# Optimization experiments

Measured on AMD Instinct MI355X. Metric: run time of the kernel, lower is better.

Reference implementation:

```python
import jax, jax.numpy as jnp
import numpy as np

N, T, D = 2, 4096, 1024
H, E, L = 8, 4, 32
DK, DV = 64, 64

def setup_inputs():
    key = jax.random.key(0)
    ks = jax.random.split(key, 8)
    def randw(k, *d):
        return jax.random.normal(k, d, dtype=jnp.float32) / np.float32(np.sqrt(d[-1]))
    return {
        "X": jax.random.normal(ks[0], (N, T, D), dtype=jnp.float32),
        "w_G": randw(ks[1], H, E, D),
        "b_G": jnp.full((H, E), -float(H) ** 0.5, dtype=jnp.float32),
        "w_K": randw(ks[2], H, DK, D),
        "w_V": randw(ks[3], H, DV, D),
        "w_Q": randw(ks[4], H, DK, D),
        "w_O": randw(ks[5], DV * H, D),
        "init_K_rec": randw(ks[6], E, L, DK),
        "init_V_rec": randw(ks[7], E, L, DV),
    }

def _pscan(A, Xv, Y0):
    # Y_t = A_t * Y_{t-1} + X_t along axis 3 (chunk index), Y_{-1} = Y0
    Ae = jnp.broadcast_to(A[..., None], Xv.shape)
    Xv = Xv.at[..., 0, :].add(A[..., 0, None] * Y0)
    def op(c1, c2):
        a1, x1 = c1
        a2, x2 = c2
        return a1 * a2, a2 * x1 + x2
    _, Y = jax.lax.associative_scan(op, (Ae, Xv), axis=3)
    return Y

def reference(X, w_G, b_G, w_K, w_V, w_Q, w_O, init_K_rec, init_V_rec):
    n, t, _ = X.shape
    t_pad = ((t - 1) // L + 1) * L
    Xp = jnp.pad(X, ((0, 0), (0, t_pad - t), (0, 0)))
    # gates and projections
    G = jax.nn.sigmoid(jnp.einsum('ntd,hed->nhet', Xp, w_G) + b_G[None, :, :, None])
    K = jnp.einsum('ntc,hdc->nhtd', Xp, w_K)
    V = jnp.einsum('ntc,hdc->nhtd', Xp, w_V)
    A = 1.0 - jnp.minimum(G.sum(axis=1), 1.0)               # [n, E, t_pad]
    gK = jnp.einsum('nhet,nhtd->netd', G, K)
    gV = jnp.einsum('nhet,nhtd->netd', G, V)
    # split time as (L, t_pad//L): outer dim L, scan over chunk index (matches torch unflatten(2,(L,-1)))
    tc = t_pad // L
    A = A.reshape(n, E, L, tc)
    gK = gK.reshape(n, E, L, tc, DK)
    gV = gV.reshape(n, E, L, tc, DV)
    iK = jnp.broadcast_to(init_K_rec[None], (n, E, L, DK))
    iV = jnp.broadcast_to(init_V_rec[None], (n, E, L, DV))
    nK = _pscan(A, gK, iK).reshape(n, E, t_pad, DK)
    nV = _pscan(A, gV, iV).reshape(n, E, t_pad, DV)
    recK = jnp.concatenate([iK, nK], axis=2)                 # [n, E, L+t_pad, DK]
    recV = jnp.concatenate([iV, nV], axis=2)
    # moving window of size L ending at current position (slice starts at index 1 of rec buffer)
    idx = 1 + jnp.arange(t_pad)[:, None] + jnp.arange(L)[None, :]
    uk = recK[:, :, idx]                                     # [n, E, t_pad, L, DK]
    uv = recV[:, :, idx]                                     # [n, E, t_pad, L, DV]
    Q = jnp.einsum('ntc,hdc->nhtd', Xp, w_Q)
    scores = jnp.einsum('nhtd,netld->nhtel', Q, uk) / jnp.float32(np.sqrt(DK))
    probs = jax.nn.softmax(scores.reshape(n, H, t_pad, E * L), axis=-1).reshape(scores.shape)
    Y = jnp.einsum('nhtel,netld->nthd', probs, uv).reshape(n, t_pad, H * DV)
    return (Y @ w_O)[:, :t]
```

## Files before the change

kernel.cpp:

```cpp
#include <hip/hip_runtime.h>
#include <hip/hip_bf16.h>


using f4 = float4;
typedef __attribute__((ext_vector_type(8))) short short8;
typedef __attribute__((ext_vector_type(4))) float floatx4;

__device__ __forceinline__ ushort f2bf(float x) {
  unsigned u = __float_as_uint(x);
  u += 0x7fffu + ((u >> 16) & 1u);
  return (ushort)(u >> 16);
}
__device__ __forceinline__ unsigned pk2(float lo, float hi) {
  return (unsigned)f2bf(lo) | ((unsigned)f2bf(hi) << 16);
}

__device__ __forceinline__ void gll16(const void* g, void* l) {
  __builtin_amdgcn_global_load_lds((const __attribute__((address_space(1))) void*)g,
                                   (__attribute__((address_space(3))) void*)l, 16, 0, 0);
}

__global__ __launch_bounds__(256)
void conv_f32_bf16(const float* __restrict__ src, ushort* __restrict__ dst, int n4) {
  for (int i = blockIdx.x * blockDim.x + threadIdx.x; i < n4; i += gridDim.x * blockDim.x) {
    f4 v = ((const f4*)src)[i];
    ushort4 o; o.x = f2bf(v.x); o.y = f2bf(v.y); o.z = f2bf(v.z); o.w = f2bf(v.w);
    ((ushort4*)dst)[i] = o;
  }
}

__global__ __launch_bounds__(256)
void conv_weights(const float* __restrict__ wK, const float* __restrict__ wV,
                  const float* __restrict__ wQ, const float* __restrict__ wG,
                  ushort* __restrict__ wAll) {
  int i4 = blockIdx.x * 256 + threadIdx.x;
  int idx = i4 * 4;
  int row = idx >> 10;
  f4 v = make_float4(0.f, 0.f, 0.f, 0.f);
  if (row < 512)       v = *(const f4*)&wK[idx];
  else if (row < 1024) v = *(const f4*)&wV[idx - 524288];
  else if (row < 1536) v = *(const f4*)&wQ[idx - 1048576];
  else if (row < 1568) v = *(const f4*)&wG[idx - 1572864];
  ushort4 o; o.x = f2bf(v.x); o.y = f2bf(v.y); o.z = f2bf(v.z); o.w = f2bf(v.w);
  *(ushort4*)&wAll[idx] = o;
}

__global__ __launch_bounds__(256)
void transpose_wO(const float* __restrict__ wO, ushort* __restrict__ wObf) {
  int i = blockIdx.x * 256 + threadIdx.x;
  int n = i >> 9, k = i & 511;
  wObf[i] = f2bf(wO[(size_t)k * 1024 + n]);
}

#define PROJ_STEP(KT, WAITS, STAGE_) do {                                        \
  asm volatile("s_waitcnt vmcnt(" WAITS ")" ::: "memory");                       \
  __builtin_amdgcn_s_barrier();                                                  \
  asm volatile("" ::: "memory");                                                 \
  if (STAGE_) {                                                                  \
    const int k2 = ((KT) + 2) * 32;                                              \
    ushort* la = &As[(((KT) + 2) & 3) * 8192 + tid * 8];                         \
    ushort* lb = &Bs[(((KT) + 2) & 3) * 8192 + tid * 8];                         \
    gll16(gA + k2, la); gll16(gA + 131072 + k2, la + 4096);                      \
    gll16(gB + k2, lb); gll16(gB + 131072 + k2, lb + 4096);                      \
  }                                                                              \
  {                                                                              \
    const int ko = ((KT) & 3) * 8192;                                            \
    short8 bfrag[4];                                                             \
    _Pragma("unroll")                                                            \
    for (int ni = 0; ni < 4; ni++)                                               \
      bfrag[ni] = *(const short8*)(Bf + ko + ni * 512);                          \
    __builtin_amdgcn_s_setprio(1);                                               \
    _Pragma("unroll")                                                            \
    for (int mi = 0; mi < 8; mi++) {                                             \
      short8 afrag = *(const short8*)(Af + ko + mi * 512);                       \
      _Pragma("unroll")                                                          \
      for (int ni = 0; ni < 4; ni++)                                             \
        acc[mi][ni] = __builtin_amdgcn_mfma_f32_16x16x32_bf16(                   \
            afrag, bfrag[ni], acc[mi][ni], 0, 0, 0);                             \
    }                                                                            \
    __builtin_amdgcn_s_setprio(0);                                               \
  }                                                                              \
} while (0)

__global__ __launch_bounds__(512, 2)
void proj_gemm_256(const ushort* __restrict__ Xbf, const ushort* __restrict__ wAll,
                   float* __restrict__ Kp, float* __restrict__ Vp,
                   ushort* __restrict__ Qbf, float* __restrict__ Glin)
{
  __shared__ ushort As[4 * 8192];
  __shared__ ushort Bs[4 * 8192];

  const int tid = threadIdx.x;
  const int bid = blockIdx.x;
  const int xcd = bid & 7, slot = bid >> 3;
  const int ct = slot % 7;
  const int my = xcd * 4 + slot / 7;
  const int m0 = my * 256;
  const int n0 = ct * 256;

  const int lane = tid & 63;
  const int w = tid >> 6;
  const int wm = (w >> 2) * 128;
  const int wn = (w & 3) * 64;
  const int l15 = lane & 15, lg = lane >> 4;

  const int srow = tid >> 2, sc8 = (tid & 3) * 8;
  const ushort* gA = Xbf  + (size_t)(m0 + srow) * 1024 + sc8;
  const ushort* gB = wAll + (size_t)(n0 + srow) * 1024 + sc8;

  const ushort* Af = As + (wm + l15) * 32 + lg * 8;
  const ushort* Bf = Bs + (wn + l15) * 32 + lg * 8;

  floatx4 acc[8][4];
#pragma unroll
  for (int mi = 0; mi < 8; mi++)
#pragma unroll
    for (int ni = 0; ni < 4; ni++) acc[mi][ni] = (floatx4){0.f, 0.f, 0.f, 0.f};

#pragma unroll
  for (int t_ = 0; t_ < 2; t_++) {
    const int k0 = t_ * 32;
    ushort* la = &As[t_ * 8192 + tid * 8];
    ushort* lb = &Bs[t_ * 8192 + tid * 8];
    gll16(gA + k0, la); gll16(gA + 131072 + k0, la + 4096);
    gll16(gB + k0, lb); gll16(gB + 131072 + k0, lb + 4096);
  }

#pragma unroll 1
  for (int kt = 0; kt < 30; ++kt) PROJ_STEP(kt, "4", true);
  PROJ_STEP(30, "4", false);
  PROJ_STEP(31, "0", false);

#pragma unroll
  for (int mi = 0; mi < 8; mi++) {
    const int rm = m0 + wm + mi * 16 + lg * 4;
#pragma unroll
    for (int ni = 0; ni < 4; ni++) {
      const int cn = wn + ni * 16 + l15;
#pragma unroll
      for (int j = 0; j < 4; j++) {
        const float v = acc[mi][ni][j];
        if (ct < 2)      Kp [(size_t)(rm + j) * 512 + ct * 256 + cn] = v;
        else if (ct < 4) Vp [(size_t)(rm + j) * 512 + (ct - 2) * 256 + cn] = v;
        else if (ct < 6) Qbf[(size_t)(rm + j) * 512 + (ct - 4) * 256 + cn] = f2bf(v * 0.125f);
        else if (cn < 32) Glin[(size_t)(rm + j) * 32 + cn] = v;
      }
    }
  }
}

__global__ __launch_bounds__(256)
void out_gemm_mfma(const ushort* __restrict__ Ybf, const ushort* __restrict__ wObf,
                   float* __restrict__ out)
{
  __shared__ ushort As[4096];
  __shared__ ushort Bs[4096];
  const int tid = threadIdx.x;
  const int m0 = blockIdx.y * 128;
  const int n0 = blockIdx.x * 128;
  const int lane = tid & 63;
  const int wv = tid >> 6;
  const int wm = (wv >> 1) * 64, wn = (wv & 1) * 64;

  const int srow = tid >> 2, scol = (tid & 3) * 8;
  const ushort* gA = Ybf  + (size_t)(m0 + srow) * 512 + scol;
  const ushort* gB = wObf + (size_t)(n0 + srow) * 512 + scol;
  ushort* lA0 = &As[tid * 8]; ushort* lA1 = &As[2048 + tid * 8];
  ushort* lB0 = &Bs[tid * 8]; ushort* lB1 = &Bs[2048 + tid * 8];

  floatx4 acc[4][4];
#pragma unroll
  for (int i = 0; i < 4; i++)
#pragma unroll
    for (int j = 0; j < 4; j++) acc[i][j] = (floatx4){0.f, 0.f, 0.f, 0.f};

  const int fr = lane & 15;
  const int fk = (lane >> 4) * 8;
  const short8* pA[4]; const short8* pB[4];
#pragma unroll
  for (int i = 0; i < 4; i++) {
    pA[i] = (const short8*)&As[(wm + i * 16 + fr) * 32 + fk];
    pB[i] = (const short8*)&Bs[(wn + i * 16 + fr) * 32 + fk];
  }

  for (int k0 = 0; k0 < 512; k0 += 32) {
    gll16(gA + k0, lA0);
    gll16(gA + 32768 + k0, lA1);
    gll16(gB + k0, lB0);
    gll16(gB + 32768 + k0, lB1);
    __syncthreads();
    short8 a[4], b[4];
#pragma unroll
    for (int i = 0; i < 4; i++) { a[i] = *pA[i]; b[i] = *pB[i]; }
#pragma unroll
    for (int mi = 0; mi < 4; mi++)
#pragma unroll
      for (int ni = 0; ni < 4; ni++)
        acc[mi][ni] = __builtin_amdgcn_mfma_f32_16x16x32_bf16(a[mi], b[ni], acc[mi][ni], 0, 0, 0);
    __syncthreads();
  }

  const int fq = lane >> 4;
#pragma unroll
  for (int mi = 0; mi < 4; mi++) {
    int rm = m0 + wm + mi * 16 + fq * 4;
#pragma unroll
    for (int ni = 0; ni < 4; ni++) {
      int cn = n0 + wn + ni * 16 + fr;
#pragma unroll
      for (int j = 0; j < 4; j++)
        out[(size_t)(rm + j) * 1024 + cn] = acc[mi][ni][j];
    }
  }
}

__global__ __launch_bounds__(256)
void gate_kernel(const float* __restrict__ Glin, const float* __restrict__ bG,
                 const float* __restrict__ Kp, const float* __restrict__ Vp,
                 float* __restrict__ gK, float* __restrict__ gV, float* __restrict__ Aout)
{
  const int nt = blockIdx.x * 4 + (threadIdx.x >> 6);
  const int lane = threadIdx.x & 63;
  const int n = nt >> 12;
  const int t = nt & 4095;

  float g[32];
  float gsum[4] = {0.f, 0.f, 0.f, 0.f};
#pragma unroll
  for (int f = 0; f < 32; f++) {
    float z = Glin[(size_t)nt * 32 + f] + bG[f];
    float s = 1.f / (1.f + __expf(-z));
    g[f] = s;
    gsum[f & 3] += s;
  }
  if (lane < 4) {
    float a = 1.f - fminf(gsum[lane], 1.f);
    Aout[(size_t)(n * 4 + lane) * 4096 + t] = a;
  }
  float gk[4] = {0.f, 0.f, 0.f, 0.f}, gv[4] = {0.f, 0.f, 0.f, 0.f};
#pragma unroll
  for (int h = 0; h < 8; h++) {
    float kv = Kp[(size_t)nt * 512 + h * 64 + lane];
    float vv = Vp[(size_t)nt * 512 + h * 64 + lane];
#pragma unroll
    for (int e = 0; e < 4; e++) {
      gk[e] = fmaf(g[h * 4 + e], kv, gk[e]);
      gv[e] = fmaf(g[h * 4 + e], vv, gv[e]);
    }
  }
#pragma unroll
  for (int e = 0; e < 4; e++) {
    size_t base = ((size_t)(n * 4 + e) * 4096 + t) * 64 + lane;
    gK[base] = gk[e];
    gV[base] = gv[e];
  }
}

__global__ __launch_bounds__(64)
void scan_kernel(float* __restrict__ gK, float* __restrict__ gV,
                 const float* __restrict__ Aarr,
                 const float* __restrict__ initK, const float* __restrict__ initV)
{
  __shared__ float sB[128 * 64];
  __shared__ float sA[128];
  const int b = blockIdx.x;
  const int half = b >> 8, sub = b & 255;
  float* gX = half ? gV : gK;
  const float* initX = half ? initV : initK;
  const int n = sub >> 7, r = sub & 127, e = r >> 5, l = r & 31;
  const int tbase = l * 128;
  const size_t base = ((size_t)(n * 4 + e) * 4096 + tbase) * 64;
  const int tid = threadIdx.x;

  const f4* src = (const f4*)&gX[base];
#pragma unroll
  for (int q = 0; q < 32; q++)
    *(f4*)&sB[(tid + q * 64) * 4] = src[tid + q * 64];
  sA[tid]      = Aarr[(size_t)(n * 4 + e) * 4096 + tbase + tid];
  sA[64 + tid] = Aarr[(size_t)(n * 4 + e) * 4096 + tbase + 64 + tid];
  __syncthreads();

  float state = initX[((size_t)e * 32 + l) * 64 + tid];
  float* dst = &gX[base];
  for (int c = 0; c < 128; c++) {
    state = fmaf(sA[c], state, sB[c * 64 + tid]);
    dst[c * 64 + tid] = state;
  }
}

__global__ __launch_bounds__(256, 1)
void attn_mfma(const ushort* __restrict__ Qbf, const float* __restrict__ nK,
               const float* __restrict__ nV, const float* __restrict__ initK,
               const float* __restrict__ initV, ushort* __restrict__ Yout)
{
  __shared__ ushort Kw[4][4096];
  __shared__ ushort Vt[4][4096];
  __shared__ ushort Pl[4][4096];

  const int blk = blockIdx.x;
  const int n = blk >> 7, c = blk & 127;
  const int t0 = c * 32;
  const int tid = threadIdx.x;
  const int lane = tid & 63;
  const int w = tid >> 6;
  const int l15 = lane & 15, lg = lane >> 4;

  short8 qf[4][2];
#pragma unroll
  for (int mi = 0; mi < 4; mi++) {
    int m = w * 64 + mi * 16 + l15;
    int t = t0 + (m & 31), h = m >> 5;
    const ushort* src = &Qbf[((size_t)(n * 4096 + t)) * 512 + h * 64];
#pragma unroll
    for (int kk = 0; kk < 2; kk++)
      qf[mi][kk] = *(const short8*)&src[kk * 32 + lg * 8];
  }

#pragma unroll 4
  for (int it = 0; it < 16; it++) {
    int idx = it * 256 + tid;
    int e = idx >> 10, u = (idx >> 4) & 63, d = (idx & 15) * 4;
    int s = t0 - 31 + u;
    int scl = s < 4095 ? s : 4095;
    const float* pK = (s >= 0) ? &nK[(((size_t)(n * 4 + e)) * 4096 + scl) * 64 + d]
                               : &initK[((size_t)e * 32 + (s + 32)) * 64 + d];
    const float* pV = (s >= 0) ? &nV[(((size_t)(n * 4 + e)) * 4096 + scl) * 64 + d]
                               : &initV[((size_t)e * 32 + (s + 32)) * 64 + d];
    f4 kv = *(const f4*)pK;
    f4 vv = *(const f4*)pV;
    if (u == 63) { kv = make_float4(0.f,0.f,0.f,0.f); vv = make_float4(0.f,0.f,0.f,0.f); }
    uint2 kp; kp.x = pk2(kv.x, kv.y); kp.y = pk2(kv.z, kv.w);
    int ka = (u * 128 + d * 2) ^ ((u & 7) << 4);
    *(uint2*)((char*)&Kw[e][0] + ka) = kp;
    ushort vb[4] = { f2bf(vv.x), f2bf(vv.y), f2bf(vv.z), f2bf(vv.w) };
#pragma unroll
    for (int q = 0; q < 4; q++) {
      int dq = d + q;
      int va = (dq * 128 + u * 2) ^ ((dq & 7) << 4);
      *(ushort*)((char*)&Vt[e][0] + va) = vb[q];
    }
  }
  __syncthreads();

  floatx4 Yacc[4][4];
#pragma unroll
  for (int mi = 0; mi < 4; mi++)
#pragma unroll
    for (int nd = 0; nd < 4; nd++) Yacc[mi][nd] = (floatx4){0.f,0.f,0.f,0.f};
  float mrun[4][4], lrun[4][4];
#pragma unroll
  for (int mi = 0; mi < 4; mi++)
#pragma unroll
    for (int r = 0; r < 4; r++) { mrun[mi][r] = -1e30f; lrun[mi][r] = 0.f; }

  const floatx4 zf = (floatx4){0.f,0.f,0.f,0.f};
  char* pb = (char*)&Pl[w][0];

#pragma unroll
  for (int half = 0; half < 2; half++) {
    floatx4 S[2][4][4];
#pragma unroll
    for (int ep = 0; ep < 2; ep++) {
      const int e = half * 2 + ep;
#pragma unroll
      for (int ni = 0; ni < 4; ni++) {
        const int urow = ni * 16 + l15;
        const int sw = (urow & 7) << 4;
        short8 kf0 = *(const short8*)((const char*)&Kw[e][0] + ((urow * 128 + lg * 16) ^ sw));
        short8 kf1 = *(const short8*)((const char*)&Kw[e][0] + ((urow * 128 + 64 + lg * 16) ^ sw));
#pragma unroll
        for (int mi = 0; mi < 4; mi++) {
          floatx4 t_ = __builtin_amdgcn_mfma_f32_16x16x32_bf16(qf[mi][0], kf0, zf, 0, 0, 0);
          S[ep][mi][ni] = __builtin_amdgcn_mfma_f32_16x16x32_bf16(qf[mi][1], kf1, t_, 0, 0, 0);
        }
      }
    }
#pragma unroll
    for (int mi = 0; mi < 4; mi++)
#pragma unroll
      for (int r = 0; r < 4; r++) {
        const int iq = (mi & 1) * 16 + lg * 4 + r;
        float mx = mrun[mi][r];
#pragma unroll
        for (int ep = 0; ep < 2; ep++)
#pragma unroll
          for (int ni = 0; ni < 4; ni++) {
            const int u = ni * 16 + l15;
            float v = ((unsigned)(u - iq) < 32u) ? S[ep][mi][ni][r] : -1e30f;
            S[ep][mi][ni][r] = v;
            mx = fmaxf(mx, v);
          }
        mx = fmaxf(mx, __shfl_xor(mx, 1));
        mx = fmaxf(mx, __shfl_xor(mx, 2));
        mx = fmaxf(mx, __shfl_xor(mx, 4));
        mx = fmaxf(mx, __shfl_xor(mx, 8));
        float sc = __expf(mrun[mi][r] - mx);
        mrun[mi][r] = mx;
        float sum = 0.f;
#pragma unroll
        for (int ep = 0; ep < 2; ep++)
#pragma unroll
          for (int ni = 0; ni < 4; ni++) {
            float p = __expf(S[ep][mi][ni][r] - mx);
            S[ep][mi][ni][r] = p;
            sum += p;
          }
        sum += __shfl_xor(sum, 1);
        sum += __shfl_xor(sum, 2);
        sum += __shfl_xor(sum, 4);
        sum += __shfl_xor(sum, 8);
        lrun[mi][r] = lrun[mi][r] * sc + sum;
#pragma unroll
        for (int nd = 0; nd < 4; nd++) Yacc[mi][nd][r] *= sc;
      }
#pragma unroll
    for (int ep = 0; ep < 2; ep++) {
      const int e = half * 2 + ep;
#pragma unroll
      for (int mi = 0; mi < 4; mi++)
#pragma unroll
        for (int r = 0; r < 4; r++) {
          const int m = mi * 16 + lg * 4 + r;
          const int base = m * 128, sw = (m & 7) << 4;
#pragma unroll
          for (int ni = 0; ni < 4; ni++) {
            const int u = ni * 16 + l15;
            *(ushort*)(pb + ((base + u * 2) ^ sw)) = f2bf(S[ep][mi][ni][r]);
          }
        }
      asm volatile("s_waitcnt lgkmcnt(0)" ::: "memory");
      __builtin_amdgcn_sched_barrier(0);
#pragma unroll
      for (int kk = 0; kk < 2; kk++) {
        short8 pa[4];
#pragma unroll
        for (int mi = 0; mi < 4; mi++) {
          const int m = mi * 16 + l15;
          pa[mi] = *(const short8*)(pb + ((m * 128 + kk * 64 + lg * 16) ^ ((m & 7) << 4)));
        }
#pragma unroll
        for (int nd = 0; nd < 4; nd++) {
          const int dr = nd * 16 + l15;
          short8 vf = *(const short8*)((const char*)&Vt[e][0] +
                        ((dr * 128 + kk * 64 + lg * 16) ^ ((dr & 7) << 4)));
#pragma unroll
          for (int mi = 0; mi < 4; mi++)
            Yacc[mi][nd] = __builtin_amdgcn_mfma_f32_16x16x32_bf16(pa[mi], vf, Yacc[mi][nd], 0, 0, 0);
        }
      }
    }
  }

#pragma unroll
  for (int mi = 0; mi < 4; mi++)
#pragma unroll
    for (int r = 0; r < 4; r++) {
      const float inv = 1.f / lrun[mi][r];
      const int m = w * 64 + mi * 16 + lg * 4 + r;
      const int t = t0 + (m & 31), h = m >> 5;
      ushort* dst = &Yout[((size_t)(n * 4096 + t)) * 512 + h * 64];
#pragma unroll
      for (int nd = 0; nd < 4; nd++)
        dst[nd * 16 + l15] = f2bf(Yacc[mi][nd][r] * inv);
    }
}

extern "C" void kernel_launch(void* const* d_in, const int* in_sizes, int n_in,
                              void* d_out, int out_size, void* d_ws, size_t ws_size,
                              hipStream_t stream) {
  const float* X     = (const float*)d_in[0];
  const float* wG    = (const float*)d_in[1];
  const float* bG    = (const float*)d_in[2];
  const float* wK    = (const float*)d_in[3];
  const float* wV    = (const float*)d_in[4];
  const float* wQ    = (const float*)d_in[5];
  const float* wO    = (const float*)d_in[6];
  const float* initK = (const float*)d_in[7];
  const float* initV = (const float*)d_in[8];
  float* out = (float*)d_out;

  float* ws = (float*)d_ws;
  ushort* Xbf  = (ushort*)(ws + 0);
  float*  gK   = ws + 0;
  float*  gV   = ws + 2097152;
  ushort* wAll = (ushort*)(ws + 4194304);
  ushort* wObf = (ushort*)(ws + 5111808);
  float*  Glin = ws + 5373952;
  float*  Kp   = ws + 5636096;
  ushort* Ybf  = (ushort*)Kp;
  float*  Vp   = ws + 9830400;
  ushort* Qbf  = (ushort*)(ws + 14024704);
  float*  Aarr = ws + 16121856;

  conv_f32_bf16<<<2048, 256, 0, stream>>>(X, Xbf, 2097152);
  conv_weights<<<1792, 256, 0, stream>>>(wK, wV, wQ, wG, wAll);
  transpose_wO<<<2048, 256, 0, stream>>>(wO, wObf);
  proj_gemm_256<<<224, 512, 0, stream>>>(Xbf, wAll, Kp, Vp, Qbf, Glin);
  gate_kernel<<<2048, 256, 0, stream>>>(Glin, bG, Kp, Vp, gK, gV, Aarr);
  scan_kernel<<<512, 64, 0, stream>>>(gK, gV, Aarr, initK, initV);
  attn_mfma<<<256, 256, 0, stream>>>(Qbf, gK, gV, initK, initV, Ybf);
  out_gemm_mfma<<<dim3(8, 64), 256, 0, stream>>>(Ybf, wObf, out);
}
```

Baseline: 222.9 us.

## Deepen projection prefetch to three stages and rewrite output GEMM pipelined

The projection GEMM now prefetches three k-tiles ahead instead of two, using the fourth LDS buffer, with adjusted vmcnt waits. The output GEMM is replaced by a 256x128-tile, 512-thread kernel with a four-buffer global_load_lds pipeline, an XCD-aware block-to-tile mapping and a single barrier per step. Both changes aim to hide global-memory latency behind MFMA work. The cost is more LDS per block and more in-flight loads, which may reduce occupancy.

```diff
diff --git a/kernel.cpp b/kernel.cpp
--- a/kernel.cpp
+++ b/kernel.cpp
@@ -55,13 +55,12 @@
 #define PROJ_STEP(KT, WAITS, STAGE_) do {                                        \
   asm volatile("s_waitcnt vmcnt(" WAITS ")" ::: "memory");                       \
   __builtin_amdgcn_s_barrier();                                                  \
-  asm volatile("" ::: "memory");                                                 \
   if (STAGE_) {                                                                  \
-    const int k2 = ((KT) + 2) * 32;                                              \
-    ushort* la = &As[(((KT) + 2) & 3) * 8192 + tid * 8];                         \
-    ushort* lb = &Bs[(((KT) + 2) & 3) * 8192 + tid * 8];                         \
-    gll16(gA + k2, la); gll16(gA + 131072 + k2, la + 4096);                      \
-    gll16(gB + k2, lb); gll16(gB + 131072 + k2, lb + 4096);                      \
+    const int k3 = ((KT) + 3) * 32;                                              \
+    ushort* la = &As[(((KT) + 3) & 3) * 8192 + tid * 8];                         \
+    ushort* lb = &Bs[(((KT) + 3) & 3) * 8192 + tid * 8];                         \
+    gll16(gA + k3, la); gll16(gA + 131072 + k3, la + 4096);                      \
+    gll16(gB + k3, lb); gll16(gB + 131072 + k3, lb + 4096);                      \
   }                                                                              \
   {                                                                              \
     const int ko = ((KT) & 3) * 8192;                                            \
@@ -118,7 +117,7 @@
     for (int ni = 0; ni < 4; ni++) acc[mi][ni] = (floatx4){0.f, 0.f, 0.f, 0.f};
 
 #pragma unroll
-  for (int t_ = 0; t_ < 2; t_++) {
+  for (int t_ = 0; t_ < 3; t_++) {
     const int k0 = t_ * 32;
     ushort* la = &As[t_ * 8192 + tid * 8];
     ushort* lb = &Bs[t_ * 8192 + tid * 8];
@@ -127,7 +126,8 @@
   }
 
 #pragma unroll 1
-  for (int kt = 0; kt < 30; ++kt) PROJ_STEP(kt, "4", true);
+  for (int kt = 0; kt < 29; ++kt) PROJ_STEP(kt, "8", true);
+  PROJ_STEP(29, "8", false);
   PROJ_STEP(30, "4", false);
   PROJ_STEP(31, "0", false);
 
@@ -149,64 +149,91 @@
   }
 }
 
-__global__ __launch_bounds__(256)
-void out_gemm_mfma(const ushort* __restrict__ Ybf, const ushort* __restrict__ wObf,
-                   float* __restrict__ out)
+#define OUT_STEP(KT, WAITS, STAGE_) do {                                         \
+  asm volatile("s_waitcnt vmcnt(" WAITS ")" ::: "memory");                       \
+  __builtin_amdgcn_s_barrier();                                                  \
+  if (STAGE_) {                                                                  \
+    const int k3 = ((KT) + 3) * 32;                                              \
+    ushort* la = &As[(((KT) + 3) & 3) * 8192 + tid * 8];                         \
+    ushort* lb = &Bs[(((KT) + 3) & 3) * 4096 + tid * 8];                         \
+    gll16(gA + k3, la); gll16(gA + 65536 + k3, la + 4096);                       \
+    gll16(gB + k3, lb);                                                          \
+  }                                                                              \
+  {                                                                              \
+    const int koA = ((KT) & 3) * 8192;                                           \
+    const int koB = ((KT) & 3) * 4096;                                           \
+    short8 bfrag[4];                                                             \
+    _Pragma("unroll")                                                            \
+    for (int ni = 0; ni < 4; ni++)                                               \
+      bfrag[ni] = *(const short8*)(Bf + koB + ni * 512);                         \
+    __builtin_amdgcn_s_setprio(1);                                               \
+    _Pragma("unroll")                                                            \
+    for (int mi = 0; mi < 4; mi++) {                                             \
+      short8 afrag = *(const short8*)(Af + koA + mi * 512);                      \
+      _Pragma("unroll")                                                          \
+      for (int ni = 0; ni < 4; ni++)                                             \
+        acc[mi][ni] = __builtin_amdgcn_mfma_f32_16x16x32_bf16(                   \
+            afrag, bfrag[ni], acc[mi][ni], 0, 0, 0);                             \
+    }                                                                            \
+    __builtin_amdgcn_s_setprio(0);                                               \
+  }                                                                              \
+} while (0)
+
+__global__ __launch_bounds__(512, 2)
+void out_gemm_256(const ushort* __restrict__ Ybf, const ushort* __restrict__ wObf,
+                  float* __restrict__ out)
 {
-  __shared__ ushort As[4096];
-  __shared__ ushort Bs[4096];
+  __shared__ ushort As[4 * 8192];
+  __shared__ ushort Bs[4 * 4096];
+
   const int tid = threadIdx.x;
-  const int m0 = blockIdx.y * 128;
-  const int n0 = blockIdx.x * 128;
+  const int bid = blockIdx.x;
+  const int xcd = bid & 7, slot = bid >> 3;
+  const int ct = slot & 7;
+  const int my = xcd * 4 + (slot >> 3);
+  const int m0 = my * 256;
+  const int n0 = ct * 128;
+
   const int lane = tid & 63;
-  const int wv = tid >> 6;
-  const int wm = (wv >> 1) * 64, wn = (wv & 1) * 64;
-
-  const int srow = tid >> 2, scol = (tid & 3) * 8;
-  const ushort* gA = Ybf  + (size_t)(m0 + srow) * 512 + scol;
-  const ushort* gB = wObf + (size_t)(n0 + srow) * 512 + scol;
-  ushort* lA0 = &As[tid * 8]; ushort* lA1 = &As[2048 + tid * 8];
-  ushort* lB0 = &Bs[tid * 8]; ushort* lB1 = &Bs[2048 + tid * 8];
+  const int w = tid >> 6;
+  const int wm = (w >> 1) * 64;
+  const int wn = (w & 1) * 64;
+  const int l15 = lane & 15, lg = lane >> 4;
+
+  const int srow = tid >> 2, sc8 = (tid & 3) * 8;
+  const ushort* gA = Ybf  + (size_t)(m0 + srow) * 512 + sc8;
+  const ushort* gB = wObf + (size_t)(n0 + srow) * 512 + sc8;
+
+  const ushort* Af = As + (wm + l15) * 32 + lg * 8;
+  const ushort* Bf = Bs + (wn + l15) * 32 + lg * 8;
 
   floatx4 acc[4][4];
 #pragma unroll
-  for (int i = 0; i < 4; i++)
-#pragma unroll
-    for (int j = 0; j < 4; j++) acc[i][j] = (floatx4){0.f, 0.f, 0.f, 0.f};
-
-  const int fr = lane & 15;
-  const int fk = (lane >> 4) * 8;
-  const short8* pA[4]; const short8* pB[4];
-#pragma unroll
-  for (int i = 0; i < 4; i++) {
-    pA[i] = (const short8*)&As[(wm + i * 16 + fr) * 32 + fk];
-    pB[i] = (const short8*)&Bs[(wn + i * 16 + fr) * 32 + fk];
-  }
-
-  for (int k0 = 0; k0 < 512; k0 += 32) {
-    gll16(gA + k0, lA0);
-    gll16(gA + 32768 + k0, lA1);
-    gll16(gB + k0, lB0);
-    gll16(gB + 32768 + k0, lB1);
-    __syncthreads();
-    short8 a[4], b[4];
-#pragma unroll
-    for (int i = 0; i < 4; i++) { a[i] = *pA[i]; b[i] = *pB[i]; }
-#pragma unroll
-    for (int mi = 0; mi < 4; mi++)
-#pragma unroll
-      for (int ni = 0; ni < 4; ni++)
-        acc[mi][ni] = __builtin_amdgcn_mfma_f32_16x16x32_bf16(a[mi], b[ni], acc[mi][ni], 0, 0, 0);
-    __syncthreads();
-  }
-
-  const int fq = lane >> 4;
+  for (int mi = 0; mi < 4; mi++)
+#pragma unroll
+    for (int ni = 0; ni < 4; ni++) acc[mi][ni] = (floatx4){0.f, 0.f, 0.f, 0.f};
+
+#pragma unroll
+  for (int t_ = 0; t_ < 3; t_++) {
+    const int k0 = t_ * 32;
+    ushort* la = &As[t_ * 8192 + tid * 8];
+    ushort* lb = &Bs[t_ * 4096 + tid * 8];
+    gll16(gA + k0, la); gll16(gA + 65536 + k0, la + 4096);
+    gll16(gB + k0, lb);
+  }
+
+#pragma unroll 1
+  for (int kt = 0; kt < 13; ++kt) OUT_STEP(kt, "6", true);
+  OUT_STEP(13, "6", false);
+  OUT_STEP(14, "3", false);
+  OUT_STEP(15, "0", false);
+
 #pragma unroll
   for (int mi = 0; mi < 4; mi++) {
-    int rm = m0 + wm + mi * 16 + fq * 4;
+    const int rm = m0 + wm + mi * 16 + lg * 4;
 #pragma unroll
     for (int ni = 0; ni < 4; ni++) {
-      int cn = n0 + wn + ni * 16 + fr;
+      const int cn = n0 + wn + ni * 16 + l15;
 #pragma unroll
       for (int j = 0; j < 4; j++)
         out[(size_t)(rm + j) * 1024 + cn] = acc[mi][ni][j];
@@ -499,5 +526,5 @@
   gate_kernel<<<2048, 256, 0, stream>>>(Glin, bG, Kp, Vp, gK, gV, Aarr);
   scan_kernel<<<512, 64, 0, stream>>>(gK, gV, Aarr, initK, initV);
   attn_mfma<<<256, 256, 0, stream>>>(Qbf, gK, gV, initK, initV, Ybf);
-  out_gemm_mfma<<<dim3(8, 64), 256, 0, stream>>>(Ybf, wObf, out);
-}
+  out_gemm_256<<<256, 512, 0, stream>>>(Ybf, wObf, out);
+}
```

Result: no change. 222.6 us (-0.1%).

## Retile projection and output GEMMs to 128x128 with swizzled LDS and triple buffering

Applied to the files above, without the earlier changes.

Replaces the 256x256-tile projection GEMM with a 128x128-tile version: N is padded to 1664 so 832 blocks fill the device, and conv_weights is shrunk to match. Both GEMMs now stage tiles into LDS with an XOR chunk swizzle to avoid bank conflicts, and use a 3-stage global_load_lds pipeline with one barrier per k-step. The output GEMM gains XCD-aware block mapping and software pipelining, where before it had two syncs per step and no prefetch. Smaller tiles lower the arithmetic intensity per block, but in exchange they improve occupancy and load balance and waste less padding (1792 to 1664 columns).

```diff
diff --git a/kernel.cpp b/kernel.cpp
--- a/kernel.cpp
+++ b/kernel.cpp
@@ -52,161 +52,155 @@
   wObf[i] = f2bf(wO[(size_t)k * 1024 + n]);
 }
 
-#define PROJ_STEP(KT, WAITS, STAGE_) do {                                        \
-  asm volatile("s_waitcnt vmcnt(" WAITS ")" ::: "memory");                       \
-  __builtin_amdgcn_s_barrier();                                                  \
-  asm volatile("" ::: "memory");                                                 \
-  if (STAGE_) {                                                                  \
-    const int k2 = ((KT) + 2) * 32;                                              \
-    ushort* la = &As[(((KT) + 2) & 3) * 8192 + tid * 8];                         \
-    ushort* lb = &Bs[(((KT) + 2) & 3) * 8192 + tid * 8];                         \
-    gll16(gA + k2, la); gll16(gA + 131072 + k2, la + 4096);                      \
-    gll16(gB + k2, lb); gll16(gB + 131072 + k2, lb + 4096);                      \
-  }                                                                              \
-  {                                                                              \
-    const int ko = ((KT) & 3) * 8192;                                            \
-    short8 bfrag[4];                                                             \
-    _Pragma("unroll")                                                            \
-    for (int ni = 0; ni < 4; ni++)                                               \
-      bfrag[ni] = *(const short8*)(Bf + ko + ni * 512);                          \
-    __builtin_amdgcn_s_setprio(1);                                               \
-    _Pragma("unroll")                                                            \
-    for (int mi = 0; mi < 8; mi++) {                                             \
-      short8 afrag = *(const short8*)(Af + ko + mi * 512);                       \
-      _Pragma("unroll")                                                          \
-      for (int ni = 0; ni < 4; ni++)                                             \
-        acc[mi][ni] = __builtin_amdgcn_mfma_f32_16x16x32_bf16(                   \
-            afrag, bfrag[ni], acc[mi][ni], 0, 0, 0);                             \
-    }                                                                            \
-    __builtin_amdgcn_s_setprio(0);                                               \
-  }                                                                              \
+#define GSTEP(LDA_, WAITS, STAGE_, KT) do {                                       \
+  asm volatile("s_waitcnt vmcnt(" WAITS ")" ::: "memory");                        \
+  __builtin_amdgcn_s_barrier();                                                   \
+  if (STAGE_) {                                                                   \
+    const ushort* ga = gA + (size_t)((KT) + 2) * 32;                              \
+    const ushort* gb = gB + (size_t)((KT) + 2) * 32;                              \
+    ushort* la = As + ss * 4096 + tid * 8;                                        \
+    ushort* lb = Bs + ss * 4096 + tid * 8;                                        \
+    gll16(ga, la); gll16(ga + 64 * (LDA_), la + 2048);                            \
+    gll16(gb, lb); gll16(gb + 64 * (LDA_), lb + 2048);                            \
+  }                                                                               \
+  {                                                                               \
+    const ushort* Afp = As + cs * 4096 + (wm + l15) * 32 + koff;                  \
+    const ushort* Bfp = Bs + cs * 4096 + (wn + l15) * 32 + koff;                  \
+    short8 bf_[4];                                                                \
+    _Pragma("unroll")                                                             \
+    for (int ni = 0; ni < 4; ni++) bf_[ni] = *(const short8*)(Bfp + ni * 512);    \
+    __builtin_amdgcn_s_setprio(1);                                                \
+    _Pragma("unroll")                                                             \
+    for (int mi = 0; mi < 4; mi++) {                                              \
+      short8 af_ = *(const short8*)(Afp + mi * 512);                              \
+      _Pragma("unroll")                                                           \
+      for (int ni = 0; ni < 4; ni++)                                              \
+        acc[mi][ni] = __builtin_amdgcn_mfma_f32_16x16x32_bf16(                    \
+            af_, bf_[ni], acc[mi][ni], 0, 0, 0);                                  \
+    }                                                                             \
+    __builtin_amdgcn_s_setprio(0);                                                \
+    cs = (cs == 2) ? 0 : cs + 1;                                                  \
+    ss = (ss == 2) ? 0 : ss + 1;                                                  \
+  }                                                                               \
 } while (0)
 
-__global__ __launch_bounds__(512, 2)
-void proj_gemm_256(const ushort* __restrict__ Xbf, const ushort* __restrict__ wAll,
-                   float* __restrict__ Kp, float* __restrict__ Vp,
-                   ushort* __restrict__ Qbf, float* __restrict__ Glin)
+__global__ __launch_bounds__(256, 3)
+void proj_gemm_128s(const ushort* __restrict__ Xbf, const ushort* __restrict__ wAll,
+                    float* __restrict__ Kp, float* __restrict__ Vp,
+                    ushort* __restrict__ Qbf, float* __restrict__ Glin)
 {
-  __shared__ ushort As[4 * 8192];
-  __shared__ ushort Bs[4 * 8192];
+  __shared__ ushort As[3 * 4096];
+  __shared__ ushort Bs[3 * 4096];
 
   const int tid = threadIdx.x;
   const int bid = blockIdx.x;
   const int xcd = bid & 7, slot = bid >> 3;
-  const int ct = slot % 7;
-  const int my = xcd * 4 + slot / 7;
-  const int m0 = my * 256;
-  const int n0 = ct * 256;
-
-  const int lane = tid & 63;
-  const int w = tid >> 6;
-  const int wm = (w >> 2) * 128;
-  const int wn = (w & 3) * 64;
+  const int ct = slot % 13;
+  const int my = xcd * 8 + slot / 13;
+  const int m0 = my * 128, n0 = ct * 128;
+
+  const int lane = tid & 63, w = tid >> 6;
+  const int wm = (w >> 1) * 64, wn = (w & 1) * 64;
   const int l15 = lane & 15, lg = lane >> 4;
-
-  const int srow = tid >> 2, sc8 = (tid & 3) * 8;
-  const ushort* gA = Xbf  + (size_t)(m0 + srow) * 1024 + sc8;
-  const ushort* gB = wAll + (size_t)(n0 + srow) * 1024 + sc8;
-
-  const ushort* Af = As + (wm + l15) * 32 + lg * 8;
-  const ushort* Bf = Bs + (wn + l15) * 32 + lg * 8;
-
-  floatx4 acc[8][4];
-#pragma unroll
-  for (int mi = 0; mi < 8; mi++)
+  const int fl = (l15 & 3) ^ ((l15 >> 2) & 3);
+  const int koff = ((lg ^ fl) & 3) * 8;
+
+  const int srow = tid >> 2;
+  const int schunk = (tid & 3) ^ ((srow & 3) ^ ((srow >> 2) & 3));
+  const ushort* gA = Xbf  + (size_t)(m0 + srow) * 1024 + schunk * 8;
+  const ushort* gB = wAll + (size_t)(n0 + srow) * 1024 + schunk * 8;
+
+  floatx4 acc[4][4];
+#pragma unroll
+  for (int mi = 0; mi < 4; mi++)
 #pragma unroll
     for (int ni = 0; ni < 4; ni++) acc[mi][ni] = (floatx4){0.f, 0.f, 0.f, 0.f};
 
 #pragma unroll
   for (int t_ = 0; t_ < 2; t_++) {
-    const int k0 = t_ * 32;
-    ushort* la = &As[t_ * 8192 + tid * 8];
-    ushort* lb = &Bs[t_ * 8192 + tid * 8];
-    gll16(gA + k0, la); gll16(gA + 131072 + k0, la + 4096);
-    gll16(gB + k0, lb); gll16(gB + 131072 + k0, lb + 4096);
-  }
+    const ushort* ga = gA + t_ * 32;
+    const ushort* gb = gB + t_ * 32;
+    ushort* la = As + t_ * 4096 + tid * 8;
+    ushort* lb = Bs + t_ * 4096 + tid * 8;
+    gll16(ga, la); gll16(ga + 65536, la + 2048);
+    gll16(gb, lb); gll16(gb + 65536, lb + 2048);
+  }
+  int cs = 0, ss = 2;
 
 #pragma unroll 1
-  for (int kt = 0; kt < 30; ++kt) PROJ_STEP(kt, "4", true);
-  PROJ_STEP(30, "4", false);
-  PROJ_STEP(31, "0", false);
-
-#pragma unroll
-  for (int mi = 0; mi < 8; mi++) {
+  for (int kt = 0; kt < 31; ++kt) GSTEP(1024, "4", kt <= 29, kt);
+  GSTEP(1024, "0", false, 31);
+
+#pragma unroll
+  for (int mi = 0; mi < 4; mi++) {
     const int rm = m0 + wm + mi * 16 + lg * 4;
 #pragma unroll
     for (int ni = 0; ni < 4; ni++) {
-      const int cn = wn + ni * 16 + l15;
+      const int Cg = n0 + wn + ni * 16 + l15;
 #pragma unroll
       for (int j = 0; j < 4; j++) {
         const float v = acc[mi][ni][j];
-        if (ct < 2)      Kp [(size_t)(rm + j) * 512 + ct * 256 + cn] = v;
-        else if (ct < 4) Vp [(size_t)(rm + j) * 512 + (ct - 2) * 256 + cn] = v;
-        else if (ct < 6) Qbf[(size_t)(rm + j) * 512 + (ct - 4) * 256 + cn] = f2bf(v * 0.125f);
-        else if (cn < 32) Glin[(size_t)(rm + j) * 32 + cn] = v;
+        if (Cg < 512)        Kp [(size_t)(rm + j) * 512 + Cg] = v;
+        else if (Cg < 1024)  Vp [(size_t)(rm + j) * 512 + Cg - 512] = v;
+        else if (Cg < 1536)  Qbf[(size_t)(rm + j) * 512 + Cg - 1024] = f2bf(v * 0.125f);
+        else if (Cg < 1568)  Glin[(size_t)(rm + j) * 32 + Cg - 1536] = v;
       }
     }
   }
 }
 
-__global__ __launch_bounds__(256)
-void out_gemm_mfma(const ushort* __restrict__ Ybf, const ushort* __restrict__ wObf,
+__global__ __launch_bounds__(256, 3)
+void out_gemm_128s(const ushort* __restrict__ Ybf, const ushort* __restrict__ wObf,
                    float* __restrict__ out)
 {
-  __shared__ ushort As[4096];
-  __shared__ ushort Bs[4096];
+  __shared__ ushort As[3 * 4096];
+  __shared__ ushort Bs[3 * 4096];
+
   const int tid = threadIdx.x;
-  const int m0 = blockIdx.y * 128;
-  const int n0 = blockIdx.x * 128;
-  const int lane = tid & 63;
-  const int wv = tid >> 6;
-  const int wm = (wv >> 1) * 64, wn = (wv & 1) * 64;
-
-  const int srow = tid >> 2, scol = (tid & 3) * 8;
-  const ushort* gA = Ybf  + (size_t)(m0 + srow) * 512 + scol;
-  const ushort* gB = wObf + (size_t)(n0 + srow) * 512 + scol;
-  ushort* lA0 = &As[tid * 8]; ushort* lA1 = &As[2048 + tid * 8];
-  ushort* lB0 = &Bs[tid * 8]; ushort* lB1 = &Bs[2048 + tid * 8];
+  const int bid = blockIdx.x;
+  const int xcd = bid & 7, slot = bid >> 3;
+  const int ct = slot & 7;
+  const int my = xcd * 8 + (slot >> 3);
+  const int m0 = my * 128, n0 = ct * 128;
+
+  const int lane = tid & 63, w = tid >> 6;
+  const int wm = (w >> 1) * 64, wn = (w & 1) * 64;
+  const int l15 = lane & 15, lg = lane >> 4;
+  const int fl = (l15 & 3) ^ ((l15 >> 2) & 3);
+  const int koff = ((lg ^ fl) & 3) * 8;
+
+  const int srow = tid >> 2;
+  const int schunk = (tid & 3) ^ ((srow & 3) ^ ((srow >> 2) & 3));
+  const ushort* gA = Ybf  + (size_t)(m0 + srow) * 512 + schunk * 8;
+  const ushort* gB = wObf + (size_t)(n0 + srow) * 512 + schunk * 8;
 
   floatx4 acc[4][4];
 #pragma unroll
-  for (int i = 0; i < 4; i++)
-#pragma unroll
-    for (int j = 0; j < 4; j++) acc[i][j] = (floatx4){0.f, 0.f, 0.f, 0.f};
-
-  const int fr = lane & 15;
-  const int fk = (lane >> 4) * 8;
-  const short8* pA[4]; const short8* pB[4];
-#pragma unroll
-  for (int i = 0; i < 4; i++) {
-    pA[i] = (const short8*)&As[(wm + i * 16 + fr) * 32 + fk];
-    pB[i] = (const short8*)&Bs[(wn + i * 16 + fr) * 32 + fk];
-  }
-
-  for (int k0 = 0; k0 < 512; k0 += 32) {
-    gll16(gA + k0, lA0);
-    gll16(gA + 32768 + k0, lA1);
-    gll16(gB + k0, lB0);
-    gll16(gB + 32768 + k0, lB1);
-    __syncthreads();
-    short8 a[4], b[4];
-#pragma unroll
-    for (int i = 0; i < 4; i++) { a[i] = *pA[i]; b[i] = *pB[i]; }
-#pragma unroll
-    for (int mi = 0; mi < 4; mi++)
-#pragma unroll
-      for (int ni = 0; ni < 4; ni++)
-        acc[mi][ni] = __builtin_amdgcn_mfma_f32_16x16x32_bf16(a[mi], b[ni], acc[mi][ni], 0, 0, 0);
-    __syncthreads();
-  }
-
-  const int fq = lane >> 4;
+  for (int mi = 0; mi < 4; mi++)
+#pragma unroll
+    for (int ni = 0; ni < 4; ni++) acc[mi][ni] = (floatx4){0.f, 0.f, 0.f, 0.f};
+
+#pragma unroll
+  for (int t_ = 0; t_ < 2; t_++) {
+    const ushort* ga = gA + t_ * 32;
+    const ushort* gb = gB + t_ * 32;
+    ushort* la = As + t_ * 4096 + tid * 8;
+    ushort* lb = Bs + t_ * 4096 + tid * 8;
+    gll16(ga, la); gll16(ga + 32768, la + 2048);
+    gll16(gb, lb); gll16(gb + 32768, lb + 2048);
+  }
+  int cs = 0, ss = 2;
+
+#pragma unroll 1
+  for (int kt = 0; kt < 15; ++kt) GSTEP(512, "4", kt <= 13, kt);
+  GSTEP(512, "0", false, 15);
+
 #pragma unroll
   for (int mi = 0; mi < 4; mi++) {
-    int rm = m0 + wm + mi * 16 + fq * 4;
+    const int rm = m0 + wm + mi * 16 + lg * 4;
 #pragma unroll
     for (int ni = 0; ni < 4; ni++) {
-      int cn = n0 + wn + ni * 16 + fr;
+      const int cn = n0 + wn + ni * 16 + l15;
 #pragma unroll
       for (int j = 0; j < 4; j++)
         out[(size_t)(rm + j) * 1024 + cn] = acc[mi][ni][j];
@@ -493,11 +487,11 @@
   float*  Aarr = ws + 16121856;
 
   conv_f32_bf16<<<2048, 256, 0, stream>>>(X, Xbf, 2097152);
-  conv_weights<<<1792, 256, 0, stream>>>(wK, wV, wQ, wG, wAll);
+  conv_weights<<<1664, 256, 0, stream>>>(wK, wV, wQ, wG, wAll);
   transpose_wO<<<2048, 256, 0, stream>>>(wO, wObf);
-  proj_gemm_256<<<224, 512, 0, stream>>>(Xbf, wAll, Kp, Vp, Qbf, Glin);
+  proj_gemm_128s<<<832, 256, 0, stream>>>(Xbf, wAll, Kp, Vp, Qbf, Glin);
   gate_kernel<<<2048, 256, 0, stream>>>(Glin, bG, Kp, Vp, gK, gV, Aarr);
   scan_kernel<<<512, 64, 0, stream>>>(gK, gV, Aarr, initK, initV);
   attn_mfma<<<256, 256, 0, stream>>>(Qbf, gK, gV, initK, initV, Ybf);
-  out_gemm_mfma<<<dim3(8, 64), 256, 0, stream>>>(Ybf, wObf, out);
-}
+  out_gemm_128s<<<512, 256, 0, stream>>>(Ybf, wObf, out);
+}
```

Measured after the change: 221.1 us. No clear change (-0.8%).
